# Kernel optimization log

Measured on AMD Instinct MI355X. Metric: run time of the kernel, lower is better.

The kernel has to match this reference:

```python
import jax, jax.numpy as jnp
import numpy as np

FT_IN = 40960
VFT_IN = 640


def _sparse_linear(indices, values, W, b, B):
    # y[r] = sum_{k: row[k]==r} values[k] * W[:, col[k]]  + b
    # W: [out, in]; gather columns as rows of W.T -> [nnz, out]
    rows = indices[0]
    cols = indices[1]
    contrib = W.T[cols] * values[:, None]          # [nnz, out]
    acc = jnp.zeros((B, W.shape[0]), dtype=W.dtype).at[rows].add(contrib)
    return acc + b


def setup_inputs() -> dict:
    B = 8192
    NNZ_PER_POS = 32
    NNZ = B * NNZ_PER_POS
    FT_OUT = 256
    key = jax.random.key(0)
    ks = jax.random.split(key, 8)

    def make_indices(k):
        kb, kf = jax.random.split(k)
        bids = jax.random.randint(kb, (NNZ,), 0, B, dtype=jnp.int32)
        fids = jax.random.randint(kf, (NNZ,), 0, FT_IN, dtype=jnp.int32)
        return jnp.stack([bids, fids], axis=0)  # [2, NNZ]

    s = 1.0 / np.sqrt(FT_IN)
    sv = 1.0 / np.sqrt(VFT_IN)
    so = 1.0 / np.sqrt(2 * FT_OUT)
    return {
        "stm_indices": make_indices(ks[0]),
        "nstm_indices": make_indices(ks[1]),
        "values": jnp.ones((NNZ,), dtype=jnp.float32),
        "size": B,
        "ft_w": jax.random.uniform(ks[2], (FT_OUT, FT_IN), jnp.float32, -s, s),
        "ft_b": jax.random.uniform(ks[3], (FT_OUT,), jnp.float32, -s, s),
        "fft_w": jax.random.uniform(ks[4], (FT_OUT, VFT_IN), jnp.float32, -sv, sv),
        "fft_b": jax.random.uniform(ks[5], (FT_OUT,), jnp.float32, -sv, sv),
        "out_w": jax.random.uniform(ks[6], (1, 2 * FT_OUT), jnp.float32, -so, so),
        "out_b": jax.random.uniform(ks[7], (1,), jnp.float32, -so, so),
    }


def reference(stm_indices, nstm_indices, values, size, ft_w, ft_b, fft_w, fft_b, out_w, out_b):
    B = size
    # factorized (virtual) feature indices: column % 640
    v_stm = jnp.stack([stm_indices[0], stm_indices[1] % VFT_IN], axis=0)
    v_nstm = jnp.stack([nstm_indices[0], nstm_indices[1] % VFT_IN], axis=0)

    stm_ft = _sparse_linear(stm_indices, values, ft_w, ft_b, B) + \
             _sparse_linear(v_stm, values, fft_w, fft_b, B) - fft_b  # bias added once in torch? no:
    # NOTE: torch adds both biases (ft.bias and fft.bias); undo the subtraction above.
    stm_ft = stm_ft + fft_b
    nstm_ft = _sparse_linear(nstm_indices, values, ft_w, ft_b, B) + \
              _sparse_linear(v_nstm, values, fft_w, fft_b, B)

    hidden = jnp.clip(jnp.concatenate([stm_ft, nstm_ft], axis=1), 0.0, 1.0)  # [B, 2*ft_out]
    return jax.nn.sigmoid(hidden @ out_w.T + out_b)  # [B, 1]
```

## Files before the change

kernel.cpp:

```cpp
#include <hip/hip_runtime.h>
#include <math.h>

#define FT_OUT 256
#define VFT 640
#define CAP 96

typedef _Float16 half8_t __attribute__((ext_vector_type(8)));
typedef float    float8_t __attribute__((ext_vector_type(8)));

static __device__ __forceinline__ unsigned pack_cv(int c, float v) {
    _Float16 h = (_Float16)v;
    unsigned short b = __builtin_bit_cast(unsigned short, h);
    return ((unsigned)c << 16) | (unsigned)b;
}

__global__ __launch_bounds__(256) void prep_k(
    const float* __restrict__ ft_w, const float* __restrict__ fft_w,
    _Float16* __restrict__ W2h, int ft_in,
    const int* __restrict__ stm, const int* __restrict__ nstm,
    const float* __restrict__ vals, int nnz,
    int* __restrict__ cnt_s, int* __restrict__ cnt_n,
    unsigned* __restrict__ slot_s, unsigned* __restrict__ slot_n, int nfill)
{
    __shared__ float tile[64][65];
    if ((int)blockIdx.x < nfill) {
        int k = ((int)blockIdx.x * 256 + (int)threadIdx.x) * 2;
        if (k >= nnz) return;
        int2   rs = *(const int2*)(stm + k);
        int2   cs = *(const int2*)(stm + nnz + k);
        int2   rn = *(const int2*)(nstm + k);
        int2   cn = *(const int2*)(nstm + nnz + k);
        float2 v  = *(const float2*)(vals + k);
        unsigned e0 = pack_cv(cs.x, v.x), e1 = pack_cv(cs.y, v.y);
        unsigned e2 = pack_cv(cn.x, v.x), e3 = pack_cv(cn.y, v.y);
        int p0 = atomicAdd(&cnt_s[rs.x], 1);
        int p1 = atomicAdd(&cnt_s[rs.y], 1);
        int p2 = atomicAdd(&cnt_n[rn.x], 1);
        int p3 = atomicAdd(&cnt_n[rn.y], 1);
        if (p0 < CAP) slot_s[(size_t)rs.x * CAP + p0] = e0;
        if (p1 < CAP) slot_s[(size_t)rs.y * CAP + p1] = e1;
        if (p2 < CAP) slot_n[(size_t)rn.x * CAP + p2] = e2;
        if (p3 < CAP) slot_n[(size_t)rn.y * CAP + p3] = e3;
    } else {
        int bx = (int)blockIdx.x - nfill;
        int cb = (bx >> 2) * 64;
        int ob = (bx & 3) * 64;
        int fvb = cb % VFT;
        int tc4 = threadIdx.x & 15, tr = threadIdx.x >> 4;
#pragma unroll
        for (int i = 0; i < 4; i++) {
            int o = i * 16 + tr;
            const float4 f = *(const float4*)(ft_w + (size_t)(ob + o) * ft_in + cb + tc4 * 4);
            const float4 g = *(const float4*)(fft_w + (size_t)(ob + o) * VFT + fvb + tc4 * 4);
            tile[o][tc4 * 4 + 0] = f.x + g.x; tile[o][tc4 * 4 + 1] = f.y + g.y;
            tile[o][tc4 * 4 + 2] = f.z + g.z; tile[o][tc4 * 4 + 3] = f.w + g.w;
        }
        __syncthreads();
        int g = threadIdx.x & 7, cl = threadIdx.x >> 3;
#pragma unroll
        for (int i = 0; i < 2; i++) {
            int c = i * 32 + cl, col = cb + c;
            half8_t h;
#pragma unroll
            for (int jj = 0; jj < 8; jj++)
                h[jj] = (_Float16)tile[g * 8 + jj][c];
            *(half8_t*)(W2h + (size_t)col * FT_OUT + ob + g * 8) = h;
        }
    }
}

__global__ __launch_bounds__(256) void fused_k(const _Float16* __restrict__ W2h,
    const int* __restrict__ cnt_s, const unsigned* __restrict__ slot_s,
    const int* __restrict__ cnt_n, const unsigned* __restrict__ slot_n,
    const float* __restrict__ ft_b, const float* __restrict__ fft_b,
    const float* __restrict__ out_w, const float* __restrict__ out_b,
    float* __restrict__ out, int B) {
    int lane = threadIdx.x & 63;
    int wid  = threadIdx.x >> 6;
    int row  = blockIdx.x * 2 + (wid >> 1);
    int side = wid & 1;
    int hi   = lane >> 5;
    int sl   = lane & 31;

    const int*      cnt  = side ? cnt_n : cnt_s;
    const unsigned* slot = (side ? slot_n : slot_s) + (size_t)row * CAP;
    int n = min(cnt[row], CAP);

    float8_t acc;
#pragma unroll
    for (int k = 0; k < 8; k++) acc[k] = 0.f;
    if (hi == 0) {
        const float4* fb = (const float4*)(ft_b + sl * 8);
        const float4* gb = (const float4*)(fft_b + sl * 8);
        float4 a0 = fb[0], a1 = fb[1], c0 = gb[0], c1 = gb[1];
        acc[0] = a0.x + c0.x; acc[1] = a0.y + c0.y; acc[2] = a0.z + c0.z; acc[3] = a0.w + c0.w;
        acc[4] = a1.x + c1.x; acc[5] = a1.y + c1.y; acc[6] = a1.z + c1.z; acc[7] = a1.w + c1.w;
    }

#define PROC2(p_, q_)                                                               \
    {                                                                               \
        unsigned u_ = hi ? (q_) : (p_);                                             \
        int   c_ = (int)(u_ >> 16);                                                 \
        float v_ = (float)__builtin_bit_cast(_Float16, (unsigned short)(u_ & 0xffffu)); \
        const half8_t w_ = *(const half8_t*)(W2h + ((size_t)c_ << 8) + (sl << 3));  \
        _Pragma("unroll")                                                           \
        for (int k = 0; k < 8; k++) acc[k] += v_ * (float)w_[k];                    \
    }

    const uint4* sp4 = (const uint4*)slot;
    int j = 0;
    for (; j + 16 <= n; j += 16) {
        const uint4 a = sp4[(j >> 2) + 0];
        const uint4 b = sp4[(j >> 2) + 1];
        const uint4 c = sp4[(j >> 2) + 2];
        const uint4 d = sp4[(j >> 2) + 3];
        PROC2(a.x, a.y) PROC2(a.z, a.w)
        PROC2(b.x, b.y) PROC2(b.z, b.w)
        PROC2(c.x, c.y) PROC2(c.z, c.w)
        PROC2(d.x, d.y) PROC2(d.z, d.w)
    }
    for (; j + 4 <= n; j += 4) {
        const uint4 a = sp4[j >> 2];
        PROC2(a.x, a.y) PROC2(a.z, a.w)
    }
    if (j + 2 <= n) {
        const uint2 a = *(const uint2*)(slot + j);
        PROC2(a.x, a.y)
        j += 2;
    }
    if (j < n) {
        unsigned u = slot[j];
        int   c_ = hi ? 0 : (int)(u >> 16);
        float v_ = hi ? 0.f
                      : (float)__builtin_bit_cast(_Float16, (unsigned short)(u & 0xffffu));
        const half8_t w_ = *(const half8_t*)(W2h + ((size_t)c_ << 8) + (sl << 3));
#pragma unroll
        for (int k = 0; k < 8; k++) acc[k] += v_ * (float)w_[k];
    }
#undef PROC2

#pragma unroll
    for (int k = 0; k < 8; k++) {
        float o = __shfl_xor(acc[k], 32, 64);
        acc[k] = fminf(fmaxf(acc[k] + o, 0.f), 1.f);
    }

    const float4* ow = (const float4*)(out_w + side * FT_OUT + sl * 8);
    const float4 w0 = ow[0], w1 = ow[1];
    float p = acc[0] * w0.x + acc[1] * w0.y + acc[2] * w0.z + acc[3] * w0.w
            + acc[4] * w1.x + acc[5] * w1.y + acc[6] * w1.z + acc[7] * w1.w;
#pragma unroll
    for (int m = 32; m >= 1; m >>= 1) p += __shfl_xor(p, m, 64);
    p *= 0.5f;

    __shared__ float part[4];
    if (lane == 0) part[wid] = p;
    __syncthreads();
    if (threadIdx.x < 2) {
        float q = part[threadIdx.x * 2] + part[threadIdx.x * 2 + 1] + out_b[0];
        out[blockIdx.x * 2 + threadIdx.x] = 1.f / (1.f + __expf(-q));
    }
}

extern "C" void kernel_launch(void* const* d_in, const int* in_sizes, int n_in,
                              void* d_out, int out_size, void* d_ws, size_t ws_size,
                              hipStream_t stream) {
    const int*   stm    = (const int*)d_in[0];
    const int*   nstm   = (const int*)d_in[1];
    const float* values = (const float*)d_in[2];
    const float* ft_w   = (const float*)d_in[4];
    const float* ft_b   = (const float*)d_in[5];
    const float* fft_w  = (const float*)d_in[6];
    const float* fft_b  = (const float*)d_in[7];
    const float* out_w  = (const float*)d_in[8];
    const float* out_b  = (const float*)d_in[9];
    float* out = (float*)d_out;

    int B = out_size;
    int nnz = in_sizes[0] / 2;
    int ft_in = in_sizes[4] / FT_OUT;

    _Float16* W2h    = (_Float16*)d_ws;
    unsigned* slot_s = (unsigned*)(W2h + (size_t)ft_in * FT_OUT);
    unsigned* slot_n = slot_s + (size_t)B * CAP;
    int*      cnt_s  = (int*)(slot_n + (size_t)B * CAP);
    int*      cnt_n  = cnt_s + B;

    int nbuild = (ft_in / 64) * (FT_OUT / 64);
    int nfill  = (nnz / 2 + 255) / 256;

    hipMemsetAsync(cnt_s, 0, 2 * (size_t)B * sizeof(int), stream);
    prep_k<<<nfill + nbuild, 256, 0, stream>>>(ft_w, fft_w, W2h, ft_in,
                                               stm, nstm, values, nnz,
                                               cnt_s, cnt_n, slot_s, slot_n, nfill);
    fused_k<<<B / 2, 256, 0, stream>>>(W2h, cnt_s, slot_s, cnt_n, slot_n,
                                       ft_b, fft_b, out_w, out_b, out, B);
}
```

Before: 165.0 us.

## Pad atomic counters, use nontemporal slot stores, drop LDS transpose in weight build

Row counters are padded to a 64-byte stride so the atomics for different rows stop sharing cache lines, and bucket slot entries are written with nontemporal stores. The fused-weight build no longer transposes through shared memory: each thread owns one input column and reads 32 output rows directly with coalesced row-wise loads, writing a packed half8 run per step. This removes the shared-memory round trip and barrier, but uses more global loads per thread and a larger counter array to memset.

After: 180.5 us. 1.09x slower.

```diff
diff --git a/kernel.cpp b/kernel.cpp
--- a/kernel.cpp
+++ b/kernel.cpp
@@ -4,6 +4,7 @@
 #define FT_OUT 256
 #define VFT 640
 #define CAP 96
+#define CSTRIDE 16
 
 typedef _Float16 half8_t __attribute__((ext_vector_type(8)));
 typedef float    float8_t __attribute__((ext_vector_type(8)));
@@ -22,7 +23,6 @@
     int* __restrict__ cnt_s, int* __restrict__ cnt_n,
     unsigned* __restrict__ slot_s, unsigned* __restrict__ slot_n, int nfill)
 {
-    __shared__ float tile[64][65];
     if ((int)blockIdx.x < nfill) {
         int k = ((int)blockIdx.x * 256 + (int)threadIdx.x) * 2;
         if (k >= nnz) return;
@@ -33,38 +33,32 @@
         float2 v  = *(const float2*)(vals + k);
         unsigned e0 = pack_cv(cs.x, v.x), e1 = pack_cv(cs.y, v.y);
         unsigned e2 = pack_cv(cn.x, v.x), e3 = pack_cv(cn.y, v.y);
-        int p0 = atomicAdd(&cnt_s[rs.x], 1);
-        int p1 = atomicAdd(&cnt_s[rs.y], 1);
-        int p2 = atomicAdd(&cnt_n[rn.x], 1);
-        int p3 = atomicAdd(&cnt_n[rn.y], 1);
-        if (p0 < CAP) slot_s[(size_t)rs.x * CAP + p0] = e0;
-        if (p1 < CAP) slot_s[(size_t)rs.y * CAP + p1] = e1;
-        if (p2 < CAP) slot_n[(size_t)rn.x * CAP + p2] = e2;
-        if (p3 < CAP) slot_n[(size_t)rn.y * CAP + p3] = e3;
+        int p0 = atomicAdd(&cnt_s[rs.x * CSTRIDE], 1);
+        int p1 = atomicAdd(&cnt_s[rs.y * CSTRIDE], 1);
+        int p2 = atomicAdd(&cnt_n[rn.x * CSTRIDE], 1);
+        int p3 = atomicAdd(&cnt_n[rn.y * CSTRIDE], 1);
+        if (p0 < CAP) __builtin_nontemporal_store(e0, &slot_s[(size_t)rs.x * CAP + p0]);
+        if (p1 < CAP) __builtin_nontemporal_store(e1, &slot_s[(size_t)rs.y * CAP + p1]);
+        if (p2 < CAP) __builtin_nontemporal_store(e2, &slot_n[(size_t)rn.x * CAP + p2]);
+        if (p3 < CAP) __builtin_nontemporal_store(e3, &slot_n[(size_t)rn.y * CAP + p3]);
     } else {
-        int bx = (int)blockIdx.x - nfill;
-        int cb = (bx >> 2) * 64;
-        int ob = (bx & 3) * 64;
-        int fvb = cb % VFT;
-        int tc4 = threadIdx.x & 15, tr = threadIdx.x >> 4;
+        int bx  = (int)blockIdx.x - nfill;
+        int col = (bx >> 3) * 256 + (int)threadIdx.x;
+        int rb  = (bx & 7) * 32;
+        int fcol = col % VFT;
+        const float* fw = ft_w  + (size_t)rb * ft_in + col;
+        const float* gw = fft_w + (size_t)rb * VFT  + fcol;
+        _Float16* dst = W2h + (size_t)col * FT_OUT + rb;
 #pragma unroll
         for (int i = 0; i < 4; i++) {
-            int o = i * 16 + tr;
-            const float4 f = *(const float4*)(ft_w + (size_t)(ob + o) * ft_in + cb + tc4 * 4);
-            const float4 g = *(const float4*)(fft_w + (size_t)(ob + o) * VFT + fvb + tc4 * 4);
-            tile[o][tc4 * 4 + 0] = f.x + g.x; tile[o][tc4 * 4 + 1] = f.y + g.y;
-            tile[o][tc4 * 4 + 2] = f.z + g.z; tile[o][tc4 * 4 + 3] = f.w + g.w;
-        }
-        __syncthreads();
-        int g = threadIdx.x & 7, cl = threadIdx.x >> 3;
-#pragma unroll
-        for (int i = 0; i < 2; i++) {
-            int c = i * 32 + cl, col = cb + c;
             half8_t h;
 #pragma unroll
-            for (int jj = 0; jj < 8; jj++)
-                h[jj] = (_Float16)tile[g * 8 + jj][c];
-            *(half8_t*)(W2h + (size_t)col * FT_OUT + ob + g * 8) = h;
+            for (int j = 0; j < 8; j++) {
+                float a = fw[(size_t)(i * 8 + j) * ft_in];
+                float b = gw[(i * 8 + j) * VFT];
+                h[j] = (_Float16)(a + b);
+            }
+            *(half8_t*)(dst + i * 8) = h;
         }
     }
 }
@@ -84,7 +78,7 @@
 
     const int*      cnt  = side ? cnt_n : cnt_s;
     const unsigned* slot = (side ? slot_n : slot_s) + (size_t)row * CAP;
-    int n = min(cnt[row], CAP);
+    int n = min(cnt[row * CSTRIDE], CAP);
 
     float8_t acc;
 #pragma unroll
@@ -184,12 +178,12 @@
     unsigned* slot_s = (unsigned*)(W2h + (size_t)ft_in * FT_OUT);
     unsigned* slot_n = slot_s + (size_t)B * CAP;
     int*      cnt_s  = (int*)(slot_n + (size_t)B * CAP);
-    int*      cnt_n  = cnt_s + B;
+    int*      cnt_n  = cnt_s + (size_t)B * CSTRIDE;
 
-    int nbuild = (ft_in / 64) * (FT_OUT / 64);
+    int nbuild = (ft_in / 256) * (FT_OUT / 32);
     int nfill  = (nnz / 2 + 255) / 256;
 
-    hipMemsetAsync(cnt_s, 0, 2 * (size_t)B * sizeof(int), stream);
+    hipMemsetAsync(cnt_s, 0, 2 * (size_t)B * CSTRIDE * sizeof(int), stream);
     prep_k<<<nfill + nbuild, 256, 0, stream>>>(ft_w, fft_w, W2h, ft_in,
                                                stm, nstm, values, nnz,
                                                cnt_s, cnt_n, slot_s, slot_n, nfill);
```
